# Kernel optimization log

Measured on AMD Instinct MI355X. Metric: run time of the kernel, lower is better.

Reference implementation:

```python
import jax, jax.numpy as jnp
import numpy as np

N_NODES = 100000
N_EDGES = 1600000


def setup_inputs() -> dict:
    key = jax.random.key(0)
    k1, k2, k3, k4 = jax.random.split(key, 4)
    in_c, hid_c, out_c = 128, 128, 64
    x = jax.random.normal(k1, (N_NODES, in_c), dtype=jnp.float32)
    edge_index = jax.random.randint(k2, (2, N_EDGES), 0, N_NODES, dtype=jnp.int64)
    W1 = jax.random.normal(k3, (in_c, hid_c), dtype=jnp.float32) * (1.0 / np.sqrt(in_c))
    b1 = jnp.zeros((hid_c,), dtype=jnp.float32)
    W2 = jax.random.normal(k4, (hid_c, out_c), dtype=jnp.float32) * (1.0 / np.sqrt(hid_c))
    b2 = jnp.zeros((out_c,), dtype=jnp.float32)
    return {"x": x, "edge_index": edge_index, "W1": W1, "b1": b1, "W2": W2, "b2": b2}


def reference(x, edge_index, W1, b1, W2, b2):
    # PyG GCNConv default: add self-loops, symmetric deg normalization, bias.
    N = x.shape[0]
    loops = jnp.arange(N, dtype=edge_index.dtype)
    src = jnp.concatenate([edge_index[0], loops])  # message sources (j)
    dst = jnp.concatenate([edge_index[1], loops])  # aggregation targets (i)
    ones = jnp.ones(src.shape[0], dtype=x.dtype)
    deg = jax.ops.segment_sum(ones, dst, num_segments=N)  # in-degree incl. self-loops
    dis = jnp.where(deg > 0, jax.lax.rsqrt(deg), 0.0)     # deg^{-1/2}, inf->0
    norm = dis[src] * dis[dst]                             # [E+N]

    def gcn(h, W, b):
        h = h @ W                                  # linear transform first (fewer bytes moved)
        msg = h[src] * norm[:, None]               # gather + scale, [E+N, C]
        return jax.ops.segment_sum(msg, dst, num_segments=N) + b

    h = jax.nn.relu(gcn(x, W1, b1))
    return gcn(h, W2, b2)
```

## Files before the change

### kernel.cpp

```cpp
#include <hip/hip_runtime.h>


constexpr int SCAN_CHUNK = 4096;
constexpr int NBKT = 512;
constexpr int EPB  = 2048;
constexpr int CSR_CAP = 12288;

using short8 = __attribute__((ext_vector_type(8))) short;
using f32x4  = __attribute__((ext_vector_type(4))) float;

__device__ __forceinline__ unsigned short f2bf(float f) {
  unsigned u = __float_as_uint(f);
  unsigned r = (u + 0x7FFFu + ((u >> 16) & 1u)) >> 16;
  return (unsigned short)r;
}
__device__ __forceinline__ float bf2f(unsigned short h) {
  return __uint_as_float(((unsigned)h) << 16);
}

__device__ __forceinline__ int ld_idx(const void* ei, int is64, long long i) {
  return is64 ? (int)((const long long*)ei)[i] : ((const int*)ei)[i];
}

__device__ __forceinline__ int sniff64(const unsigned* ei, int tid) {
  unsigned v = (tid < 128) ? ei[2 * tid + 1] : 0u;
  return __syncthreads_or((int)(v != 0u)) ? 0 : 1;
}


__global__ __launch_bounds__(256) void ks_part_g(const int* __restrict__ in,
                                                 int* __restrict__ partial, int m) {
  __shared__ int red[256];
  int b = blockIdx.x, tid = threadIdx.x;
  int base = b * SCAN_CHUNK + tid * 16;
  int s = 0;
#pragma unroll
  for (int i = 0; i < 16; ++i) {
    int idx = base + i;
    if (idx < m) s += in[idx];
  }
  red[tid] = s;
  __syncthreads();
  for (int off = 128; off > 0; off >>= 1) {
    if (tid < off) red[tid] += red[tid + off];
    __syncthreads();
  }
  if (tid == 0) partial[b] = red[0];
}

__global__ __launch_bounds__(256) void ks_write_g(const int* __restrict__ in,
                                                  const int* __restrict__ partial,
                                                  int* __restrict__ out, int m) {
  __shared__ int red[256];
  __shared__ int tsum[256];
  int b = blockIdx.x, tid = threadIdx.x;
  int pb = 0;
  for (int j = tid; j < b; j += 256) pb += partial[j];
  red[tid] = pb;
  __syncthreads();
  for (int off = 128; off > 0; off >>= 1) {
    if (tid < off) red[tid] += red[tid + off];
    __syncthreads();
  }
  int block_base = red[0];
  __syncthreads();

  int base = b * SCAN_CHUNK + tid * 16;
  int vals[16];
  int s = 0;
#pragma unroll
  for (int i = 0; i < 16; ++i) {
    int idx = base + i;
    int v = (idx < m) ? in[idx] : 0;
    vals[i] = s;
    s += v;
  }
  tsum[tid] = s;
  __syncthreads();
  for (int off = 1; off < 256; off <<= 1) {
    int t = (tid >= off) ? tsum[tid - off] : 0;
    __syncthreads();
    tsum[tid] += t;
    __syncthreads();
  }
  int toff = block_base + ((tid == 0) ? 0 : tsum[tid - 1]);
#pragma unroll
  for (int i = 0; i < 16; ++i) {
    int idx = base + i;
    if (idx < m) out[idx] = toff + vals[i];
  }
}


__global__ __launch_bounds__(256) void k_hist(const void* __restrict__ ei,
                                              int* __restrict__ hist,
                                              int e, int nblk, int npb) {
  __shared__ int h[NBKT];
  int blk = blockIdx.x, tid = threadIdx.x;
  int is64 = sniff64((const unsigned*)ei, tid);
  for (int i = tid; i < NBKT; i += 256) h[i] = 0;
  __syncthreads();
  int base = blk * EPB;
  int end = base + EPB; if (end > e) end = e;
  for (int i = base + tid; i < end; i += 256) {
    int d = ld_idx(ei, is64, (long long)e + i);
    atomicAdd(&h[d / npb], 1);
  }
  __syncthreads();
  for (int i = tid; i < NBKT; i += 256)
    hist[(size_t)i * nblk + blk] = h[i];
}

__global__ __launch_bounds__(256) void k_partition(const void* __restrict__ ei,
                                                   const int* __restrict__ scanned,
                                                   unsigned* __restrict__ pairbuf,
                                                   int e, int nblk, int npb) {
  __shared__ int off[NBKT];
  int blk = blockIdx.x, tid = threadIdx.x;
  int is64 = sniff64((const unsigned*)ei, tid);
  for (int i = tid; i < NBKT; i += 256)
    off[i] = scanned[(size_t)i * nblk + blk];
  __syncthreads();
  int base = blk * EPB;
  int end = base + EPB; if (end > e) end = e;
  for (int i = base + tid; i < end; i += 256) {
    int s = ld_idx(ei, is64, i);
    int d = ld_idx(ei, is64, (long long)e + i);
    int bkt = d / npb;
    int pos = atomicAdd(&off[bkt], 1);
    pairbuf[pos] = (unsigned)s | ((unsigned)(d - bkt * npb) << 20);
  }
}

__global__ __launch_bounds__(256) void k_bucket_all(const unsigned* __restrict__ pairbuf,
                                                    const int* __restrict__ scanned,
                                                    int* __restrict__ rowptr,
                                                    int* __restrict__ cursor,
                                                    float* __restrict__ dis,
                                                    int* __restrict__ csr,
                                                    int n, int e, int npb, int nblk) {
  __shared__ int lcsr[CSR_CAP];
  __shared__ int cnt[256];
  __shared__ int scn[256];
  int b = blockIdx.x, tid = threadIdx.x;
  if (b == 0 && tid == 0) rowptr[n] = e;
  int lo = b * npb;
  if (lo >= n) return;
  int hi = lo + npb; if (hi > n) hi = n;
  int nn = hi - lo;
  int seg_base = scanned[(size_t)b * nblk];
  int seg_end  = (b == NBKT - 1) ? e : scanned[(size_t)(b + 1) * nblk];
  int cnt_total = seg_end - seg_base;

  for (int i = tid; i < nn; i += 256) cnt[i] = 0;
  __syncthreads();
  for (int i = tid; i < cnt_total; i += 256)
    atomicAdd(&cnt[pairbuf[seg_base + i] >> 20], 1);
  __syncthreads();

  int v = (tid < nn) ? cnt[tid] : 0;
  scn[tid] = v;
  __syncthreads();
  for (int off = 1; off < 256; off <<= 1) {
    int t = (tid >= off) ? scn[tid - off] : 0;
    __syncthreads();
    scn[tid] += t;
    __syncthreads();
  }
  int start = (tid == 0) ? 0 : scn[tid - 1];
  if (tid < nn) {
    int node = lo + tid;
    rowptr[node] = seg_base + start;
    cursor[node] = seg_base + start;
    dis[node] = rsqrtf((float)(v + 1));
  }
  __syncthreads();
  if (tid < nn) cnt[tid] = start;
  __syncthreads();

  if (cnt_total <= CSR_CAP) {
    for (int i = tid; i < cnt_total; i += 256) {
      unsigned p = pairbuf[seg_base + i];
      int q = atomicAdd(&cnt[p >> 20], 1);
      lcsr[q] = (int)(p & 0xFFFFFu);
    }
    __syncthreads();
    for (int i = tid; i < cnt_total; i += 256) csr[seg_base + i] = lcsr[i];
  } else {
    for (int i = tid; i < cnt_total; i += 256) {
      unsigned p = pairbuf[seg_base + i];
      int q = atomicAdd(&cursor[lo + (int)(p >> 20)], 1);
      csr[q] = (int)(p & 0xFFFFFu);
    }
  }
}

template <int NCOL, bool XBF16>
__global__ __launch_bounds__(256) void k_gemm_mfma(const void* __restrict__ Xv,
                                                   const float* __restrict__ W,
                                                   const float* __restrict__ dis,
                                                   unsigned short* __restrict__ S,
                                                   int nrows) {
  constexpr int ROWS = 64;
  constexpr int NCF = NCOL / 16;
  __shared__ __align__(16) unsigned short xs[ROWS * 128];
  __shared__ __align__(16) unsigned short wt[NCOL * 128];
  int tid = threadIdx.x;

  for (int id = tid; id < 128 * NCOL; id += 256) {
    int k = id / NCOL, c = id % NCOL;
    wt[(c * 128 + k) ^ ((c & 7) << 3)] = f2bf(W[id]);
  }

  int wv = tid >> 6, lane = tid & 63;
  int l16 = lane & 15, lk = lane >> 4;
  int arow = wv * 16 + l16;
  int npass = (nrows + ROWS - 1) / ROWS;

  for (int p = blockIdx.x; p < npass; p += gridDim.x) {
    int r0 = p * ROWS;
    __syncthreads();
#pragma unroll
    for (int it = 0; it < 4; ++it) {
      int id = tid + 256 * it;
      int row = id >> 4, kc = id & 15;
      int gr = r0 + row;
      unsigned short v[8];
      if (gr < nrows) {
        if (XBF16) {
          const unsigned short* xb = (const unsigned short*)Xv + (size_t)gr * 128 + kc * 8;
#pragma unroll
          for (int j = 0; j < 8; ++j) v[j] = xb[j];
        } else {
          const float4* x4 = (const float4*)Xv + (size_t)gr * 32 + kc * 2;
          float4 f0 = x4[0], f1 = x4[1];
          v[0] = f2bf(f0.x); v[1] = f2bf(f0.y); v[2] = f2bf(f0.z); v[3] = f2bf(f0.w);
          v[4] = f2bf(f1.x); v[5] = f2bf(f1.y); v[6] = f2bf(f1.z); v[7] = f2bf(f1.w);
        }
      } else {
#pragma unroll
        for (int j = 0; j < 8; ++j) v[j] = 0;
      }
      int idx = (row * 128 + kc * 8) ^ ((row & 7) << 3);
      *(short8*)&xs[idx] = *(short8*)v;
    }
    __syncthreads();

    short8 a[4];
#pragma unroll
    for (int ks = 0; ks < 4; ++ks)
      a[ks] = *(short8*)&xs[(arow * 128 + ks * 32 + lk * 8) ^ ((arow & 7) << 3)];

    f32x4 acc[NCF];
#pragma unroll
    for (int cf = 0; cf < NCF; ++cf) acc[cf] = (f32x4){0.f, 0.f, 0.f, 0.f};

#pragma unroll
    for (int cf = 0; cf < NCF; ++cf) {
      int col = cf * 16 + l16;
#pragma unroll
      for (int ks = 0; ks < 4; ++ks) {
        short8 bfr = *(short8*)&wt[(col * 128 + ks * 32 + lk * 8) ^ ((col & 7) << 3)];
        acc[cf] = __builtin_amdgcn_mfma_f32_16x16x32_bf16(a[ks], bfr, acc[cf], 0, 0, 0);
      }
    }

#pragma unroll
    for (int r = 0; r < 4; ++r) {
      int gr = r0 + wv * 16 + lk * 4 + r;
      if (gr < nrows) {
        float dv = dis[gr];
#pragma unroll
        for (int cf = 0; cf < NCF; ++cf)
          S[(size_t)gr * NCOL + cf * 16 + l16] = f2bf(acc[cf][r] * dv);
      }
    }
  }
}

__global__ __launch_bounds__(256) void k_agg1(const unsigned short* __restrict__ S,
                                              const int* __restrict__ rowptr,
                                              const int* __restrict__ csr,
                                              const float* __restrict__ dis,
                                              const float* __restrict__ b1,
                                              unsigned short* __restrict__ H, int n) {
  int node = blockIdx.x * 4 + (threadIdx.x >> 6);
  if (node >= n) return;
  int lane = threadIdx.x & 63;
  int eg = lane >> 4;
  int cp = lane & 15;
  float acc[8];
  if (eg == 0) {
    short8 v = *(const short8*)&S[(size_t)node * 128 + cp * 8];
#pragma unroll
    for (int k = 0; k < 8; ++k) acc[k] = bf2f((unsigned short)v[k]);
  } else {
#pragma unroll
    for (int k = 0; k < 8; ++k) acc[k] = 0.f;
  }
  int2 rp = *(const int2*)&rowptr[node];
  int e = rp.x + eg;
  for (; e + 4 < rp.y; e += 8) {
    int j0 = csr[e], j1 = csr[e + 4];
    short8 v0 = *(const short8*)&S[(size_t)j0 * 128 + cp * 8];
    short8 v1 = *(const short8*)&S[(size_t)j1 * 128 + cp * 8];
#pragma unroll
    for (int k = 0; k < 8; ++k)
      acc[k] += bf2f((unsigned short)v0[k]) + bf2f((unsigned short)v1[k]);
  }
  if (e < rp.y) {
    int j = csr[e];
    short8 v = *(const short8*)&S[(size_t)j * 128 + cp * 8];
#pragma unroll
    for (int k = 0; k < 8; ++k) acc[k] += bf2f((unsigned short)v[k]);
  }
#pragma unroll
  for (int k = 0; k < 8; ++k) {
    acc[k] += __shfl_xor(acc[k], 16);
    acc[k] += __shfl_xor(acc[k], 32);
  }
  if (eg == 0) {
    float d = dis[node];
    float4 bb0 = ((const float4*)b1)[cp * 2];
    float4 bb1 = ((const float4*)b1)[cp * 2 + 1];
    float bv[8] = {bb0.x, bb0.y, bb0.z, bb0.w, bb1.x, bb1.y, bb1.z, bb1.w};
    short8 o;
#pragma unroll
    for (int k = 0; k < 8; ++k)
      o[k] = (short)f2bf(fmaxf(fmaf(acc[k], d, bv[k]), 0.f));
    *(short8*)&H[(size_t)node * 128 + cp * 8] = o;
  }
}

__global__ __launch_bounds__(256) void k_agg2(const unsigned short* __restrict__ S,
                                              const int* __restrict__ rowptr,
                                              const int* __restrict__ csr,
                                              const float* __restrict__ dis,
                                              const float* __restrict__ b2,
                                              float* __restrict__ O, int n) {
  int node = blockIdx.x * 4 + (threadIdx.x >> 6);
  if (node >= n) return;
  int lane = threadIdx.x & 63;
  int eg = lane >> 3;
  int cp = lane & 7;
  float acc[8];
  if (eg == 0) {
    short8 v = *(const short8*)&S[(size_t)node * 64 + cp * 8];
#pragma unroll
    for (int k = 0; k < 8; ++k) acc[k] = bf2f((unsigned short)v[k]);
  } else {
#pragma unroll
    for (int k = 0; k < 8; ++k) acc[k] = 0.f;
  }
  int2 rp = *(const int2*)&rowptr[node];
  int e = rp.x + eg;
  for (; e + 8 < rp.y; e += 16) {
    int j0 = csr[e], j1 = csr[e + 8];
    short8 v0 = *(const short8*)&S[(size_t)j0 * 64 + cp * 8];
    short8 v1 = *(const short8*)&S[(size_t)j1 * 64 + cp * 8];
#pragma unroll
    for (int k = 0; k < 8; ++k)
      acc[k] += bf2f((unsigned short)v0[k]) + bf2f((unsigned short)v1[k]);
  }
  if (e < rp.y) {
    int j = csr[e];
    short8 v = *(const short8*)&S[(size_t)j * 64 + cp * 8];
#pragma unroll
    for (int k = 0; k < 8; ++k) acc[k] += bf2f((unsigned short)v[k]);
  }
#pragma unroll
  for (int k = 0; k < 8; ++k) {
    acc[k] += __shfl_xor(acc[k], 8);
    acc[k] += __shfl_xor(acc[k], 16);
    acc[k] += __shfl_xor(acc[k], 32);
  }
  if (eg == 0) {
    float d = dis[node];
    float4 bb0 = ((const float4*)b2)[cp * 2];
    float4 bb1 = ((const float4*)b2)[cp * 2 + 1];
    float bv[8] = {bb0.x, bb0.y, bb0.z, bb0.w, bb1.x, bb1.y, bb1.z, bb1.w};
    float4 o0, o1;
    o0.x = fmaf(acc[0], d, bv[0]); o0.y = fmaf(acc[1], d, bv[1]);
    o0.z = fmaf(acc[2], d, bv[2]); o0.w = fmaf(acc[3], d, bv[3]);
    o1.x = fmaf(acc[4], d, bv[4]); o1.y = fmaf(acc[5], d, bv[5]);
    o1.z = fmaf(acc[6], d, bv[6]); o1.w = fmaf(acc[7], d, bv[7]);
    ((float4*)O)[(size_t)node * 16 + cp * 2] = o0;
    ((float4*)O)[(size_t)node * 16 + cp * 2 + 1] = o1;
  }
}

extern "C" void kernel_launch(void* const* d_in, const int* in_sizes, int n_in,
                              void* d_out, int out_size, void* d_ws, size_t ws_size,
                              hipStream_t stream) {
  const float* x  = (const float*)d_in[0];
  const void*  ei = d_in[1];
  const float* W1 = (const float*)d_in[2];
  const float* b1 = (const float*)d_in[3];
  const float* W2 = (const float*)d_in[4];
  const float* b2 = (const float*)d_in[5];
  float* out = (float*)d_out;

  const int N = in_sizes[0] / 128;
  const int E = in_sizes[1] / 2;
  const int npb  = (N + NBKT - 1) / NBKT;
  const int nblk = (E + EPB - 1) / EPB;
  const int m    = NBKT * nblk;

  char* w = (char*)d_ws;
  size_t off = 0;
  auto alloc = [&](size_t bytes) -> void* {
    void* p = (void*)(w + off);
    off += (bytes + 255) & ~(size_t)255;
    return p;
  };
  int*            rowptr  = (int*)alloc((size_t)(N + 1) * 4);
  int*            cursor  = (int*)alloc((size_t)N * 4);
  float*          dis     = (float*)alloc((size_t)N * 4);
  int*            csr     = (int*)alloc((size_t)E * 4);
  unsigned*       pairbuf = (unsigned*)alloc((size_t)E * 4);
  int*            hist    = (int*)alloc((size_t)m * 4);
  int*            scanned = (int*)alloc((size_t)m * 4);
  unsigned short* s1      = (unsigned short*)alloc((size_t)N * 128 * 2);
  unsigned short* s2      = (unsigned short*)alloc((size_t)N * 64 * 2);
  unsigned short* h       = (unsigned short*)alloc((size_t)N * 128 * 2);
  int*            partial = (int*)alloc(256 * 4);

  int npartsM = (m + SCAN_CHUNK - 1) / SCAN_CHUNK;

  k_hist<<<nblk, 256, 0, stream>>>(ei, hist, E, nblk, npb);
  ks_part_g<<<npartsM, 256, 0, stream>>>(hist, partial, m);
  ks_write_g<<<npartsM, 256, 0, stream>>>(hist, partial, scanned, m);
  k_partition<<<nblk, 256, 0, stream>>>(ei, scanned, pairbuf, E, nblk, npb);
  k_bucket_all<<<NBKT, 256, 0, stream>>>(pairbuf, scanned, rowptr, cursor, dis, csr,
                                         N, E, npb, nblk);

  k_gemm_mfma<128, false><<<1024, 256, 0, stream>>>(x, W1, dis, s1, N);
  k_agg1<<<(N + 3) / 4, 256, 0, stream>>>(s1, rowptr, csr, dis, b1, h, N);
  k_gemm_mfma<64, true><<<1024, 256, 0, stream>>>(h, W2, dis, s2, N);
  k_agg2<<<(N + 3) / 4, 256, 0, stream>>>(s2, rowptr, csr, dis, b2, out, N);
}
```

Before: 205.1 us.

## Fuse CSR build stages into one cooperative kernel with grid syncs

Replaces the five separate CSR-construction launches (histogram, two scan passes, partition, bucket) with a single cooperative kernel of 512 blocks that uses grid.sync between phases. EPB is doubled so the histogram and partition phases need no more blocks than the 512-block grid. The goal is to remove kernel launch gaps and tail effects in the preprocessing stage. In exchange it depends on every block being co-resident, and the large shared allocation could limit occupancy. If the cooperative launch fails, it falls back to the old multi-kernel path.

```diff
diff --git a/kernel.cpp b/kernel.cpp
--- a/kernel.cpp
+++ b/kernel.cpp
@@ -1,9 +1,12 @@
 #include <hip/hip_runtime.h>
+#include <hip/hip_cooperative_groups.h>
+
+namespace cg = cooperative_groups;
 
 
 constexpr int SCAN_CHUNK = 4096;
 constexpr int NBKT = 512;
-constexpr int EPB  = 2048;
+constexpr int EPB  = 4096;
 constexpr int CSR_CAP = 12288;
 
 using short8 = __attribute__((ext_vector_type(8))) short;
@@ -25,6 +28,167 @@
 __device__ __forceinline__ int sniff64(const unsigned* ei, int tid) {
   unsigned v = (tid < 128) ? ei[2 * tid + 1] : 0u;
   return __syncthreads_or((int)(v != 0u)) ? 0 : 1;
+}
+
+__global__ __launch_bounds__(256) void k_prep(const void* __restrict__ ei,
+                                              int* __restrict__ hist,
+                                              int* __restrict__ partial,
+                                              int* __restrict__ scanned,
+                                              unsigned* __restrict__ pairbuf,
+                                              int* __restrict__ rowptr,
+                                              int* __restrict__ cursor,
+                                              float* __restrict__ dis,
+                                              int* __restrict__ csr,
+                                              int n, int e, int npb, int nblk,
+                                              int m, int nparts) {
+  cg::grid_group grid = cg::this_grid();
+  __shared__ int smem[CSR_CAP];
+  __shared__ int cnt[256];
+  __shared__ int scn[256];
+  int b = blockIdx.x, tid = threadIdx.x;
+  int is64 = sniff64((const unsigned*)ei, tid);
+
+  if (b < nblk) {
+    for (int i = tid; i < NBKT; i += 256) smem[i] = 0;
+    __syncthreads();
+    int base = b * EPB;
+    int end = base + EPB; if (end > e) end = e;
+    for (int i = base + tid; i < end; i += 256) {
+      int d = ld_idx(ei, is64, (long long)e + i);
+      atomicAdd(&smem[d / npb], 1);
+    }
+    __syncthreads();
+    for (int i = tid; i < NBKT; i += 256)
+      hist[(size_t)i * nblk + b] = smem[i];
+  }
+  __threadfence();
+  grid.sync();
+
+  if (b < nparts) {
+    int base = b * SCAN_CHUNK + tid * 16;
+    int s = 0;
+#pragma unroll
+    for (int i = 0; i < 16; ++i) {
+      int idx = base + i;
+      if (idx < m) s += hist[idx];
+    }
+    cnt[tid] = s;
+    __syncthreads();
+    for (int off = 128; off > 0; off >>= 1) {
+      if (tid < off) cnt[tid] += cnt[tid + off];
+      __syncthreads();
+    }
+    if (tid == 0) partial[b] = cnt[0];
+  }
+  __threadfence();
+  grid.sync();
+
+  if (b < nparts) {
+    int pb = 0;
+    for (int j = tid; j < b; j += 256) pb += partial[j];
+    cnt[tid] = pb;
+    __syncthreads();
+    for (int off = 128; off > 0; off >>= 1) {
+      if (tid < off) cnt[tid] += cnt[tid + off];
+      __syncthreads();
+    }
+    int block_base = cnt[0];
+    __syncthreads();
+    int base = b * SCAN_CHUNK + tid * 16;
+    int vals[16];
+    int s = 0;
+#pragma unroll
+    for (int i = 0; i < 16; ++i) {
+      int idx = base + i;
+      int v = (idx < m) ? hist[idx] : 0;
+      vals[i] = s;
+      s += v;
+    }
+    scn[tid] = s;
+    __syncthreads();
+    for (int off = 1; off < 256; off <<= 1) {
+      int t = (tid >= off) ? scn[tid - off] : 0;
+      __syncthreads();
+      scn[tid] += t;
+      __syncthreads();
+    }
+    int toff = block_base + ((tid == 0) ? 0 : scn[tid - 1]);
+#pragma unroll
+    for (int i = 0; i < 16; ++i) {
+      int idx = base + i;
+      if (idx < m) scanned[idx] = toff + vals[i];
+    }
+  }
+  __threadfence();
+  grid.sync();
+
+  if (b < nblk) {
+    for (int i = tid; i < NBKT; i += 256)
+      smem[i] = scanned[(size_t)i * nblk + b];
+    __syncthreads();
+    int base = b * EPB;
+    int end = base + EPB; if (end > e) end = e;
+    for (int i = base + tid; i < end; i += 256) {
+      int s = ld_idx(ei, is64, i);
+      int d = ld_idx(ei, is64, (long long)e + i);
+      int bkt = d / npb;
+      int pos = atomicAdd(&smem[bkt], 1);
+      pairbuf[pos] = (unsigned)s | ((unsigned)(d - bkt * npb) << 20);
+    }
+  }
+  __threadfence();
+  grid.sync();
+
+  if (b == 0 && tid == 0) rowptr[n] = e;
+  int lo = b * npb;
+  if (lo >= n) return;
+  int hi = lo + npb; if (hi > n) hi = n;
+  int nn = hi - lo;
+  int seg_base = scanned[(size_t)b * nblk];
+  int seg_end  = (b == NBKT - 1) ? e : scanned[(size_t)(b + 1) * nblk];
+  int cnt_total = seg_end - seg_base;
+
+  for (int i = tid; i < nn; i += 256) cnt[i] = 0;
+  __syncthreads();
+  for (int i = tid; i < cnt_total; i += 256)
+    atomicAdd(&cnt[pairbuf[seg_base + i] >> 20], 1);
+  __syncthreads();
+
+  int v = (tid < nn) ? cnt[tid] : 0;
+  scn[tid] = v;
+  __syncthreads();
+  for (int off = 1; off < 256; off <<= 1) {
+    int t = (tid >= off) ? scn[tid - off] : 0;
+    __syncthreads();
+    scn[tid] += t;
+    __syncthreads();
+  }
+  int start = (tid == 0) ? 0 : scn[tid - 1];
+  if (tid < nn) {
+    int node = lo + tid;
+    rowptr[node] = seg_base + start;
+    cursor[node] = seg_base + start;
+    dis[node] = rsqrtf((float)(v + 1));
+  }
+  __syncthreads();
+  if (tid < nn) cnt[tid] = start;
+  __syncthreads();
+
+  if (cnt_total <= CSR_CAP) {
+    for (int i = tid; i < cnt_total; i += 256) {
+      unsigned p = pairbuf[seg_base + i];
+      int q = atomicAdd(&cnt[p >> 20], 1);
+      smem[q] = (int)(p & 0xFFFFFu);
+    }
+    __syncthreads();
+    for (int i = tid; i < cnt_total; i += 256) csr[seg_base + i] = smem[i];
+  } else {
+    for (int i = tid; i < cnt_total; i += 256) {
+      unsigned p = pairbuf[seg_base + i];
+      int q = atomicAdd(&cursor[lo + (int)(p >> 20)], 1);
+      csr[q] = (int)(p & 0xFFFFFu);
+    }
+  }
 }
 
 
@@ -64,7 +228,6 @@
   }
   int block_base = red[0];
   __syncthreads();
-
   int base = b * SCAN_CHUNK + tid * 16;
   int vals[16];
   int s = 0;
@@ -90,7 +253,6 @@
     if (idx < m) out[idx] = toff + vals[i];
   }
 }
-
 
 __global__ __launch_bounds__(256) void k_hist(const void* __restrict__ ei,
                                               int* __restrict__ hist,
@@ -425,14 +587,23 @@
   unsigned short* h       = (unsigned short*)alloc((size_t)N * 128 * 2);
   int*            partial = (int*)alloc(256 * 4);
 
-  int npartsM = (m + SCAN_CHUNK - 1) / SCAN_CHUNK;
-
-  k_hist<<<nblk, 256, 0, stream>>>(ei, hist, E, nblk, npb);
-  ks_part_g<<<npartsM, 256, 0, stream>>>(hist, partial, m);
-  ks_write_g<<<npartsM, 256, 0, stream>>>(hist, partial, scanned, m);
-  k_partition<<<nblk, 256, 0, stream>>>(ei, scanned, pairbuf, E, nblk, npb);
-  k_bucket_all<<<NBKT, 256, 0, stream>>>(pairbuf, scanned, rowptr, cursor, dis, csr,
-                                         N, E, npb, nblk);
+  int nparts = (m + SCAN_CHUNK - 1) / SCAN_CHUNK;
+
+  int N_ = N, E_ = E, npb_ = npb, nblk_ = nblk, m_ = m, nparts_ = nparts;
+  void* args[] = {(void*)&ei, (void*)&hist, (void*)&partial, (void*)&scanned,
+                  (void*)&pairbuf, (void*)&rowptr, (void*)&cursor, (void*)&dis,
+                  (void*)&csr, (void*)&N_, (void*)&E_, (void*)&npb_,
+                  (void*)&nblk_, (void*)&m_, (void*)&nparts_};
+  hipError_t cerr = hipLaunchCooperativeKernel((void*)k_prep, dim3(NBKT), dim3(256),
+                                               args, 0, stream);
+  if (cerr != hipSuccess) {
+    k_hist<<<nblk, 256, 0, stream>>>(ei, hist, E, nblk, npb);
+    ks_part_g<<<nparts, 256, 0, stream>>>(hist, partial, m);
+    ks_write_g<<<nparts, 256, 0, stream>>>(hist, partial, scanned, m);
+    k_partition<<<nblk, 256, 0, stream>>>(ei, scanned, pairbuf, E, nblk, npb);
+    k_bucket_all<<<NBKT, 256, 0, stream>>>(pairbuf, scanned, rowptr, cursor, dis,
+                                           csr, N, E, npb, nblk);
+  }
 
   k_gemm_mfma<128, false><<<1024, 256, 0, stream>>>(x, W1, dis, s1, N);
   k_agg1<<<(N + 3) / 4, 256, 0, stream>>>(s1, rowptr, csr, dis, b1, h, N);
```

Result: slower. 644.3 us (+214.1%).

## Replace per-block histogram scan with global bucket counts and atomic cursors

Applied to the files above, without the earlier changes.

The CSR build no longer writes a per-block by per-bucket histogram and runs a two-pass global scan over it. Each block instead adds its local bucket counts into a 512-entry global array, one small kernel scans that array, and the partition kernel recounts its slice locally and claims bucket ranges with global atomics. This removes two scan launches and a large histogram write and read, at the cost of re-reading destination indices in the partition kernel and an added memset. Edge order inside a bucket now depends on atomic ordering, so it is nondeterministic, which can change floating-point summation order. The edges-per-block size is also doubled.

```diff
diff --git a/kernel.cpp b/kernel.cpp
--- a/kernel.cpp
+++ b/kernel.cpp
@@ -1,9 +1,8 @@
 #include <hip/hip_runtime.h>
 
 
-constexpr int SCAN_CHUNK = 4096;
 constexpr int NBKT = 512;
-constexpr int EPB  = 2048;
+constexpr int EPB  = 4096;
 constexpr int CSR_CAP = 12288;
 
 using short8 = __attribute__((ext_vector_type(8))) short;
@@ -27,74 +26,9 @@
   return __syncthreads_or((int)(v != 0u)) ? 0 : 1;
 }
 
-
-__global__ __launch_bounds__(256) void ks_part_g(const int* __restrict__ in,
-                                                 int* __restrict__ partial, int m) {
-  __shared__ int red[256];
-  int b = blockIdx.x, tid = threadIdx.x;
-  int base = b * SCAN_CHUNK + tid * 16;
-  int s = 0;
-#pragma unroll
-  for (int i = 0; i < 16; ++i) {
-    int idx = base + i;
-    if (idx < m) s += in[idx];
-  }
-  red[tid] = s;
-  __syncthreads();
-  for (int off = 128; off > 0; off >>= 1) {
-    if (tid < off) red[tid] += red[tid + off];
-    __syncthreads();
-  }
-  if (tid == 0) partial[b] = red[0];
-}
-
-__global__ __launch_bounds__(256) void ks_write_g(const int* __restrict__ in,
-                                                  const int* __restrict__ partial,
-                                                  int* __restrict__ out, int m) {
-  __shared__ int red[256];
-  __shared__ int tsum[256];
-  int b = blockIdx.x, tid = threadIdx.x;
-  int pb = 0;
-  for (int j = tid; j < b; j += 256) pb += partial[j];
-  red[tid] = pb;
-  __syncthreads();
-  for (int off = 128; off > 0; off >>= 1) {
-    if (tid < off) red[tid] += red[tid + off];
-    __syncthreads();
-  }
-  int block_base = red[0];
-  __syncthreads();
-
-  int base = b * SCAN_CHUNK + tid * 16;
-  int vals[16];
-  int s = 0;
-#pragma unroll
-  for (int i = 0; i < 16; ++i) {
-    int idx = base + i;
-    int v = (idx < m) ? in[idx] : 0;
-    vals[i] = s;
-    s += v;
-  }
-  tsum[tid] = s;
-  __syncthreads();
-  for (int off = 1; off < 256; off <<= 1) {
-    int t = (tid >= off) ? tsum[tid - off] : 0;
-    __syncthreads();
-    tsum[tid] += t;
-    __syncthreads();
-  }
-  int toff = block_base + ((tid == 0) ? 0 : tsum[tid - 1]);
-#pragma unroll
-  for (int i = 0; i < 16; ++i) {
-    int idx = base + i;
-    if (idx < m) out[idx] = toff + vals[i];
-  }
-}
-
-
-__global__ __launch_bounds__(256) void k_hist(const void* __restrict__ ei,
-                                              int* __restrict__ hist,
-                                              int e, int nblk, int npb) {
+__global__ __launch_bounds__(256) void k_count(const void* __restrict__ ei,
+                                               int* __restrict__ bkt_cnt,
+                                               int e, int npb) {
   __shared__ int h[NBKT];
   int blk = blockIdx.x, tid = threadIdx.x;
   int is64 = sniff64((const unsigned*)ei, tid);
@@ -108,37 +42,69 @@
   }
   __syncthreads();
   for (int i = tid; i < NBKT; i += 256)
-    hist[(size_t)i * nblk + blk] = h[i];
+    if (h[i]) atomicAdd(&bkt_cnt[i], h[i]);
+}
+
+__global__ __launch_bounds__(256) void k_bases(const int* __restrict__ bkt_cnt,
+                                               int* __restrict__ bkt_base,
+                                               int* __restrict__ bkt_cursor,
+                                               int e) {
+  __shared__ int sums[256];
+  int tid = threadIdx.x;
+  int c0 = bkt_cnt[2 * tid], c1 = bkt_cnt[2 * tid + 1];
+  sums[tid] = c0 + c1;
+  __syncthreads();
+  for (int off = 1; off < 256; off <<= 1) {
+    int t = (tid >= off) ? sums[tid - off] : 0;
+    __syncthreads();
+    sums[tid] += t;
+    __syncthreads();
+  }
+  int excl = (tid == 0) ? 0 : sums[tid - 1];
+  bkt_base[2 * tid] = excl;
+  bkt_base[2 * tid + 1] = excl + c0;
+  bkt_cursor[2 * tid] = excl;
+  bkt_cursor[2 * tid + 1] = excl + c0;
+  if (tid == 255) bkt_base[NBKT] = e;
 }
 
 __global__ __launch_bounds__(256) void k_partition(const void* __restrict__ ei,
-                                                   const int* __restrict__ scanned,
+                                                   int* __restrict__ bkt_cursor,
                                                    unsigned* __restrict__ pairbuf,
-                                                   int e, int nblk, int npb) {
-  __shared__ int off[NBKT];
+                                                   int e, int npb) {
+  __shared__ int hcnt[NBKT];
   int blk = blockIdx.x, tid = threadIdx.x;
   int is64 = sniff64((const unsigned*)ei, tid);
-  for (int i = tid; i < NBKT; i += 256)
-    off[i] = scanned[(size_t)i * nblk + blk];
+  for (int i = tid; i < NBKT; i += 256) hcnt[i] = 0;
   __syncthreads();
   int base = blk * EPB;
   int end = base + EPB; if (end > e) end = e;
+  for (int i = base + tid; i < end; i += 256) {
+    int d = ld_idx(ei, is64, (long long)e + i);
+    atomicAdd(&hcnt[d / npb], 1);
+  }
+  __syncthreads();
+  for (int i = tid; i < NBKT; i += 256) {
+    int c = hcnt[i];
+    hcnt[i] = c ? atomicAdd(&bkt_cursor[i], c) : 0;
+  }
+  __syncthreads();
   for (int i = base + tid; i < end; i += 256) {
     int s = ld_idx(ei, is64, i);
     int d = ld_idx(ei, is64, (long long)e + i);
     int bkt = d / npb;
-    int pos = atomicAdd(&off[bkt], 1);
+    int pos = atomicAdd(&hcnt[bkt], 1);
     pairbuf[pos] = (unsigned)s | ((unsigned)(d - bkt * npb) << 20);
   }
 }
 
 __global__ __launch_bounds__(256) void k_bucket_all(const unsigned* __restrict__ pairbuf,
-                                                    const int* __restrict__ scanned,
+                                                    const int* __restrict__ bkt_base,
                                                     int* __restrict__ rowptr,
                                                     int* __restrict__ cursor,
                                                     float* __restrict__ dis,
                                                     int* __restrict__ csr,
-                                                    int n, int e, int npb, int nblk) {
+                                                    int n, int e, int npb) {
   __shared__ int lcsr[CSR_CAP];
   __shared__ int cnt[256];
   __shared__ int scn[256];
@@ -148,8 +114,8 @@
   if (lo >= n) return;
   int hi = lo + npb; if (hi > n) hi = n;
   int nn = hi - lo;
-  int seg_base = scanned[(size_t)b * nblk];
-  int seg_end  = (b == NBKT - 1) ? e : scanned[(size_t)(b + 1) * nblk];
+  int seg_base = bkt_base[b];
+  int seg_end  = bkt_base[b + 1];
   int cnt_total = seg_end - seg_base;
 
   for (int i = tid; i < nn; i += 256) cnt[i] = 0;
@@ -404,7 +370,6 @@
   const int E = in_sizes[1] / 2;
   const int npb  = (N + NBKT - 1) / NBKT;
   const int nblk = (E + EPB - 1) / EPB;
-  const int m    = NBKT * nblk;
 
   char* w = (char*)d_ws;
   size_t off = 0;
@@ -413,26 +378,24 @@
     off += (bytes + 255) & ~(size_t)255;
     return p;
   };
-  int*            rowptr  = (int*)alloc((size_t)(N + 1) * 4);
-  int*            cursor  = (int*)alloc((size_t)N * 4);
-  float*          dis     = (float*)alloc((size_t)N * 4);
-  int*            csr     = (int*)alloc((size_t)E * 4);
-  unsigned*       pairbuf = (unsigned*)alloc((size_t)E * 4);
-  int*            hist    = (int*)alloc((size_t)m * 4);
-  int*            scanned = (int*)alloc((size_t)m * 4);
-  unsigned short* s1      = (unsigned short*)alloc((size_t)N * 128 * 2);
-  unsigned short* s2      = (unsigned short*)alloc((size_t)N * 64 * 2);
-  unsigned short* h       = (unsigned short*)alloc((size_t)N * 128 * 2);
-  int*            partial = (int*)alloc(256 * 4);
-
-  int npartsM = (m + SCAN_CHUNK - 1) / SCAN_CHUNK;
-
-  k_hist<<<nblk, 256, 0, stream>>>(ei, hist, E, nblk, npb);
-  ks_part_g<<<npartsM, 256, 0, stream>>>(hist, partial, m);
-  ks_write_g<<<npartsM, 256, 0, stream>>>(hist, partial, scanned, m);
-  k_partition<<<nblk, 256, 0, stream>>>(ei, scanned, pairbuf, E, nblk, npb);
-  k_bucket_all<<<NBKT, 256, 0, stream>>>(pairbuf, scanned, rowptr, cursor, dis, csr,
-                                         N, E, npb, nblk);
+  int*            rowptr     = (int*)alloc((size_t)(N + 1) * 4);
+  int*            cursor     = (int*)alloc((size_t)N * 4);
+  float*          dis        = (float*)alloc((size_t)N * 4);
+  int*            csr        = (int*)alloc((size_t)E * 4);
+  unsigned*       pairbuf    = (unsigned*)alloc((size_t)E * 4);
+  unsigned short* s1         = (unsigned short*)alloc((size_t)N * 128 * 2);
+  unsigned short* s2         = (unsigned short*)alloc((size_t)N * 64 * 2);
+  unsigned short* h          = (unsigned short*)alloc((size_t)N * 128 * 2);
+  int*            bkt_cnt    = (int*)alloc(NBKT * 4);
+  int*            bkt_base   = (int*)alloc((NBKT + 1) * 4);
+  int*            bkt_cursor = (int*)alloc(NBKT * 4);
+
+  hipMemsetAsync(bkt_cnt, 0, NBKT * 4, stream);
+  k_count<<<nblk, 256, 0, stream>>>(ei, bkt_cnt, E, npb);
+  k_bases<<<1, 256, 0, stream>>>(bkt_cnt, bkt_base, bkt_cursor, E);
+  k_partition<<<nblk, 256, 0, stream>>>(ei, bkt_cursor, pairbuf, E, npb);
+  k_bucket_all<<<NBKT, 256, 0, stream>>>(pairbuf, bkt_base, rowptr, cursor, dis,
+                                         csr, N, E, npb);
 
   k_gemm_mfma<128, false><<<1024, 256, 0, stream>>>(x, W1, dis, s1, N);
   k_agg1<<<(N + 3) / 4, 256, 0, stream>>>(s1, rowptr, csr, dis, b1, h, N);
```

New measurement: 207.9 us. About the same (+1.4%).
